# Kernel tuning notes

Measured on AMD Instinct MI355X. Metric: run time of the kernel, lower is better.

The kernel has to match this reference:

```python
import jax, jax.numpy as jnp
import numpy as np

TEMP = 0.07
BASE_TEMP = 0.07


def setup_inputs() -> dict:
    key = jax.random.key(0)
    k1, k2 = jax.random.split(key)
    B, L, D = 512, 20, 128  # batch, num_classes, feat_size
    features = jax.random.normal(k1, (B, L, D), dtype=jnp.float32)
    # contrastive features are typically L2-normalized projections
    features = features / jnp.linalg.norm(features, axis=-1, keepdims=True)
    labels = jax.random.randint(k2, (B, L), 0, 2).astype(jnp.int32)  # multi-hot
    return {"features": features, "labels": labels}


def reference(features, labels):
    # features: [B, L, D], labels: [B, L] multi-hot
    B, L, D = features.shape
    dt = features.dtype
    lab = labels.astype(dt).T                      # [L, B]
    feat = jnp.transpose(features, (1, 0, 2))      # [L, B, D]

    logits_mask = 1.0 - jnp.eye(B, dtype=dt)       # [B, B], zero diagonal
    # mask[c, i, j] = labels[i, c] * labels[j, c] * (i != j)
    mask = (lab[:, :, None] * lab[:, None, :]) * logits_mask  # [L, B, B]

    # anchor_dot_contrast[c, l, i, j] = f[l,i] . f[c,j] / T  -> exp, masked on (i,j)
    # Compute via one big N x N gram, N = L*B (same math, single GEMM).
    F = feat.reshape(L * B, D)
    E = jnp.exp((F @ F.T) / jnp.asarray(TEMP, dt)).reshape(L, B, L, B)  # E[l,i,c,j]
    tot = E.sum(axis=(0, 3))                       # [B(i), L(c)] : sum over l, all j
    diag = jnp.diagonal(E, axis1=1, axis2=3)       # [L(l), L(c), B(i)] : j == i terms
    # sum_exp_logits[c, i] = sum_{l, j != i} exp(f[l,i].f[c,j]/T)
    S = tot.T - diag.sum(axis=0)                   # [L(c), B(i)]

    # numerator[c, i, j] = f[c,i] . f[c,j] / T
    numerator = jnp.einsum('cid,cjd->cij', feat, feat) / jnp.asarray(TEMP, dt)  # [L,B,B]
    log_prob = numerator - jnp.log(S)[:, :, None]  # [L, B, B]

    mean_log_prob_pos = (mask * log_prob).sum(axis=(0, 2))  # [B]
    average = mask.sum(axis=(0, 2))                          # [B]
    average = jnp.where(average == 0, jnp.asarray(1.0, dt), average)
    mean_log_prob_pos = mean_log_prob_pos / average

    loss = -(TEMP / BASE_TEMP) * jnp.mean(mean_log_prob_pos)
    return loss
```

## Files before the change

### kernel.cpp

```cpp
#include <hip/hip_runtime.h>
#include <hip/hip_fp8.h>


#define NB 512
#define NL 20
#define NROW (NB * NL)
#define F8BYTES (NROW * 128)
#define SCALE 4.5398160f
#define TEMP_INV 14.285714285714286f

typedef float f32x4 __attribute__((ext_vector_type(4)));

static __device__ __forceinline__ unsigned char f2fp8(float x) {
  __hip_fp8_e4m3 q(x);
  return (unsigned char)q.__x;
}

static __device__ __forceinline__ float fexp2(float x) {
#if __has_builtin(__builtin_amdgcn_exp2f)
  return __builtin_amdgcn_exp2f(x);
#else
  return exp2f(x);
#endif
}

__global__ __launch_bounds__(256) void k_prep(const float* __restrict__ feat,
                                              const int* __restrict__ labels,
                                              unsigned char* __restrict__ f8,
                                              float* __restrict__ gp) {
  const int b = blockIdx.x;
  if (b < 640) {
    int t = b * 256 + threadIdx.x;
    int q = t & 15;
    int a = t >> 4;
    int l = a >> 9;
    int i = a & 511;
    const float* src = feat + (size_t)i * (NL * 128) + l * 128 + q * 8;
    float4 v0 = *(const float4*)src;
    float4 v1 = *(const float4*)(src + 4);
    unsigned long long u = 0;
    u |= (unsigned long long)f2fp8(v0.x * SCALE);
    u |= (unsigned long long)f2fp8(v0.y * SCALE) << 8;
    u |= (unsigned long long)f2fp8(v0.z * SCALE) << 16;
    u |= (unsigned long long)f2fp8(v0.w * SCALE) << 24;
    u |= (unsigned long long)f2fp8(v1.x * SCALE) << 32;
    u |= (unsigned long long)f2fp8(v1.y * SCALE) << 40;
    u |= (unsigned long long)f2fp8(v1.z * SCALE) << 48;
    u |= (unsigned long long)f2fp8(v1.w * SCALE) << 56;
    *(unsigned long long*)(f8 + (size_t)a * 128 + ((q ^ (a & 15)) << 3)) = u;
  } else {
    __shared__ float part[2][128];
    const int idx = b - 640;
    const int c = idx >> 4, grp = idx & 15;
    const int d = threadIdx.x & 127, half = threadIdx.x >> 7;
    const int i0 = grp * 32 + half * 16;
    float s = 0.f;
#pragma unroll
    for (int k = 0; k < 16; ++k) {
      int i = i0 + k;
      s += (float)labels[i * NL + c] * feat[(size_t)i * (NL * 128) + c * 128 + d];
    }
    part[half][d] = s;
    __syncthreads();
    if (half == 0) gp[(c * 16 + grp) * 128 + d] = part[0][d] + part[1][d];
  }
}

__global__ __launch_bounds__(64) void k_gram(const unsigned char* __restrict__ f8,
                                             float* __restrict__ Pr) {
  __shared__ unsigned char lds[4096];
  const int x = blockIdx.x;
  const int h = x & 1, sr = x >> 1;
  const int c = blockIdx.y;
  const int lane = threadIdx.x;
  const int fr = lane & 15, kg = lane >> 4;
  const int x8 = fr << 3;

  long af[4][4];
#pragma unroll
  for (int kk = 0; kk < 4; ++kk)
#pragma unroll
    for (int m = 0; m < 4; ++m)
      af[kk][m] = *(const long*)(f8 + (size_t)(sr * 64 + m * 16 + fr) * 128 +
                                 ((kk * 32 + kg * 8) ^ x8));

  const unsigned char* gB = f8 + ((size_t)c * 512 + h * 256) * 128 + lane * 16;
  auto stage = [&](int buf, int t) {
    const unsigned char* g = gB + t * 2048;
    unsigned char* lb = lds + buf * 2048 + lane * 16;
    __builtin_amdgcn_global_load_lds(
        (const __attribute__((address_space(1))) unsigned int*)g,
        (__attribute__((address_space(3))) unsigned int*)lb, 16, 0, 0);
    __builtin_amdgcn_global_load_lds(
        (const __attribute__((address_space(1))) unsigned int*)(g + 1024),
        (__attribute__((address_space(3))) unsigned int*)(lb + 1024), 16, 0, 0);
  };

  stage(0, 0);
  float esum[4][4] = {};

  const int d8 = sr & 7;
  const bool diagh = ((d8 >> 2) == h);
  const int td0 = (d8 & 3) * 4;

  for (int t = 0; t < 16; ++t) {
    asm volatile("" ::: "memory");
    if (t < 15) {
      stage((t + 1) & 1, t + 1);
      asm volatile("s_waitcnt vmcnt(2)" ::: "memory");
    } else {
      asm volatile("s_waitcnt vmcnt(0)" ::: "memory");
    }

    const unsigned char* lb = lds + (t & 1) * 2048;
    f32x4 acc[4] = {};
#pragma unroll
    for (int kk = 0; kk < 4; ++kk) {
      long bf = *(const long*)(lb + fr * 128 + ((kk * 32 + kg * 8) ^ x8));
#pragma unroll
      for (int m = 0; m < 4; ++m)
        acc[m] = __builtin_amdgcn_mfma_f32_16x16x32_fp8_fp8(af[kk][m], bf, acc[m], 0, 0, 0);
    }

    if (diagh && t >= td0 && t < td0 + 4) {
      const int mt = t - td0;
#pragma unroll
      for (int m = 0; m < 4; ++m)
#pragma unroll
        for (int reg = 0; reg < 4; ++reg) {
          float ex = fexp2(acc[m][reg]);
          if (m == mt && (kg * 4 + reg) == fr) ex = 0.f;
          esum[m][reg] += ex;
        }
    } else {
#pragma unroll
      for (int m = 0; m < 4; ++m)
#pragma unroll
        for (int reg = 0; reg < 4; ++reg)
          esum[m][reg] += fexp2(acc[m][reg]);
    }
  }

#pragma unroll
  for (int m = 0; m < 4; ++m)
#pragma unroll
    for (int reg = 0; reg < 4; ++reg) {
      float e = esum[m][reg];
      e += __shfl_xor(e, 1, 64); e += __shfl_xor(e, 2, 64);
      e += __shfl_xor(e, 4, 64); e += __shfl_xor(e, 8, 64);
      if (fr == 0)
        Pr[(((size_t)c * 2 + h) * 160 + sr) * 64 + m * 16 + kg * 4 + reg] = e;
    }
}

__global__ __launch_bounds__(256) void k_ws(const float* __restrict__ Pr,
                                            const float* __restrict__ feat,
                                            const float* __restrict__ gp,
                                            float* __restrict__ Slog,
                                            float* __restrict__ wnum) {
  const int b = blockIdx.x;
  if (b < 2560) {
    __shared__ float part[2][128];
    __shared__ float gsh[128];
    const int tid = threadIdx.x;
    const int c = (b * 4) >> 9;
    const int d = tid & 127, qh = tid >> 7;
    float s = 0.f;
#pragma unroll
    for (int q = 0; q < 8; ++q)
      s += gp[(c * 16 + qh * 8 + q) * 128 + d];
    part[qh][d] = s;
    __syncthreads();
    if (tid < 128) gsh[tid] = part[0][tid] + part[1][tid];
    __syncthreads();

    const int lane = tid & 63;
    const int p = b * 4 + (tid >> 6);
    const int i = p & 511;
    float2 f = *(const float2*)(feat + (size_t)i * (NL * 128) + c * 128 + lane * 2);
    float2 gv = *(const float2*)(gsh + lane * 2);
    float v = f.x * gv.x + f.y * gv.y;
#pragma unroll
    for (int sh = 1; sh < 64; sh <<= 1) v += __shfl_xor(v, sh, 64);
    if (lane == 0) wnum[p] = (v - 1.f) * TEMP_INV;
  } else {
    int idx = (b - 2560) * 256 + threadIdx.x;
    int c = idx >> 9, i = idx & 511;
    float s = 0.f;
#pragma unroll
    for (int l2 = 0; l2 < NL; ++l2) {
      const float* p2 = Pr + (((size_t)c * 2) * 160 + l2 * 8 + (i >> 6)) * 64 + (i & 63);
      s += p2[0] + p2[160 * 64];
    }
    Slog[idx] = logf(s);
  }
}

__global__ __launch_bounds__(512) void k_final(const float* __restrict__ Slog,
                                               const float* __restrict__ wnum,
                                               const int* __restrict__ labels,
                                               float* __restrict__ out) {
  __shared__ float cnt[NL];
  __shared__ float red[8];
  const int i = threadIdx.x;
  if (i < NL) cnt[i] = 0.f;
  __syncthreads();
  int lab[NL];
#pragma unroll
  for (int cI = 0; cI < NL; ++cI) lab[cI] = labels[i * NL + cI];
#pragma unroll
  for (int cI = 0; cI < NL; ++cI)
    if (lab[cI]) atomicAdd(&cnt[cI], 1.f);
  __syncthreads();
  float avg = 0.f, acc = 0.f;
#pragma unroll
  for (int cI = 0; cI < NL; ++cI) {
    if (lab[cI]) {
      float wgt = cnt[cI] - 1.f;
      avg += wgt;
      acc += wnum[cI * NB + i] - wgt * Slog[cI * NB + i];
    }
  }
  float v = acc / (avg == 0.f ? 1.f : avg);
#pragma unroll
  for (int s = 1; s < 64; s <<= 1) v += __shfl_xor(v, s, 64);
  if ((i & 63) == 0) red[i >> 6] = v;
  __syncthreads();
  if (i == 0) {
    float tot = 0.f;
#pragma unroll
    for (int k = 0; k < 8; ++k) tot += red[k];
    out[0] = -(tot / (float)NB);
  }
}

extern "C" void kernel_launch(void* const* d_in, const int* in_sizes, int n_in,
                              void* d_out, int out_size, void* d_ws, size_t ws_size,
                              hipStream_t stream) {
  const float* feat = (const float*)d_in[0];
  const int* labels = (const int*)d_in[1];
  float* out = (float*)d_out;
  unsigned char* ws = (unsigned char*)d_ws;
  unsigned char* f8 = ws;
  float* Pr = (float*)(ws + F8BYTES);
  float* gp = Pr + 20 * 2 * 160 * 64;
  float* Slog = gp + 320 * 128;
  float* wnum = Slog + NROW;

  k_prep<<<960, 256, 0, stream>>>(feat, labels, f8, gp);
  dim3 grid(320, 20);
  k_gram<<<grid, 64, 0, stream>>>(f8, Pr);
  k_ws<<<2600, 256, 0, stream>>>(Pr, feat, gp, Slog, wnum);
  k_final<<<1, 512, 0, stream>>>(Slog, wnum, labels, out);
}
```

Before: 51.07 us.

## Fuse log-sum and final reduction into ws kernel with last-block atomic finish

Moves the per-class label counts and per-sample averages into an extra prep block, and folds the Slog computation and the final loss reduction into the ws kernel. Each wave now also reduces its 40 Pr partials with shuffles. Blocks accumulate into 64 atomic buckets, and the last block to finish, found via an atomic counter, writes the output. This removes one kernel launch and the Slog/wnum round trips. In exchange it relies on atomic ordering across blocks and does redundant log work inside wavefronts.

New measurement: 96.62 us. +89.2%, slower.

```diff
diff --git a/kernel.cpp b/kernel.cpp
--- a/kernel.cpp
+++ b/kernel.cpp
@@ -8,6 +8,7 @@
 #define F8BYTES (NROW * 128)
 #define SCALE 4.5398160f
 #define TEMP_INV 14.285714285714286f
+#define WS2_BLOCKS 2560
 
 typedef float f32x4 __attribute__((ext_vector_type(4)));
 
@@ -27,7 +28,11 @@
 __global__ __launch_bounds__(256) void k_prep(const float* __restrict__ feat,
                                               const int* __restrict__ labels,
                                               unsigned char* __restrict__ f8,
-                                              float* __restrict__ gp) {
+                                              float* __restrict__ gp,
+                                              float* __restrict__ avgv,
+                                              float* __restrict__ wgtv,
+                                              float* __restrict__ buckets,
+                                              unsigned int* __restrict__ ctr) {
   const int b = blockIdx.x;
   if (b < 640) {
     int t = b * 256 + threadIdx.x;
@@ -48,7 +53,7 @@
     u |= (unsigned long long)f2fp8(v1.z * SCALE) << 48;
     u |= (unsigned long long)f2fp8(v1.w * SCALE) << 56;
     *(unsigned long long*)(f8 + (size_t)a * 128 + ((q ^ (a & 15)) << 3)) = u;
-  } else {
+  } else if (b < 960) {
     __shared__ float part[2][128];
     const int idx = b - 640;
     const int c = idx >> 4, grp = idx & 15;
@@ -63,6 +68,34 @@
     part[half][d] = s;
     __syncthreads();
     if (half == 0) gp[(c * 16 + grp) * 128 + d] = part[0][d] + part[1][d];
+  } else {
+    __shared__ float cnt[NL];
+    const int tid = threadIdx.x;
+    if (tid < NL) cnt[tid] = 0.f;
+    if (tid >= 32 && tid < 96) buckets[tid - 32] = 0.f;
+    if (tid == 96) *ctr = 0u;
+    __syncthreads();
+    int lab2[2][NL];
+#pragma unroll
+    for (int hh = 0; hh < 2; ++hh)
+#pragma unroll
+      for (int cI = 0; cI < NL; ++cI)
+        lab2[hh][cI] = labels[(tid + hh * 256) * NL + cI];
+#pragma unroll
+    for (int hh = 0; hh < 2; ++hh)
+#pragma unroll
+      for (int cI = 0; cI < NL; ++cI)
+        if (lab2[hh][cI]) atomicAdd(&cnt[cI], 1.f);
+    __syncthreads();
+#pragma unroll
+    for (int hh = 0; hh < 2; ++hh) {
+      float av = 0.f;
+#pragma unroll
+      for (int cI = 0; cI < NL; ++cI)
+        av += lab2[hh][cI] ? (cnt[cI] - 1.f) : 0.f;
+      avgv[tid + hh * 256] = av;
+    }
+    if (tid < NL) wgtv[tid] = cnt[tid] - 1.f;
   }
 }
 
@@ -153,84 +186,66 @@
     }
 }
 
-__global__ __launch_bounds__(256) void k_ws(const float* __restrict__ Pr,
-                                            const float* __restrict__ feat,
-                                            const float* __restrict__ gp,
-                                            float* __restrict__ Slog,
-                                            float* __restrict__ wnum) {
+__global__ __launch_bounds__(256) void k_ws2(const float* __restrict__ Pr,
+                                             const float* __restrict__ feat,
+                                             const float* __restrict__ gp,
+                                             const int* __restrict__ labels,
+                                             const float* __restrict__ avgv,
+                                             const float* __restrict__ wgtv,
+                                             float* __restrict__ buckets,
+                                             unsigned int* __restrict__ ctr,
+                                             float* __restrict__ out) {
+  __shared__ float part[2][128];
+  __shared__ float gsh[128];
+  __shared__ float termsh[4];
   const int b = blockIdx.x;
-  if (b < 2560) {
-    __shared__ float part[2][128];
-    __shared__ float gsh[128];
-    const int tid = threadIdx.x;
-    const int c = (b * 4) >> 9;
-    const int d = tid & 127, qh = tid >> 7;
-    float s = 0.f;
-#pragma unroll
-    for (int q = 0; q < 8; ++q)
-      s += gp[(c * 16 + qh * 8 + q) * 128 + d];
-    part[qh][d] = s;
-    __syncthreads();
-    if (tid < 128) gsh[tid] = part[0][tid] + part[1][tid];
-    __syncthreads();
-
-    const int lane = tid & 63;
-    const int p = b * 4 + (tid >> 6);
-    const int i = p & 511;
-    float2 f = *(const float2*)(feat + (size_t)i * (NL * 128) + c * 128 + lane * 2);
-    float2 gv = *(const float2*)(gsh + lane * 2);
-    float v = f.x * gv.x + f.y * gv.y;
-#pragma unroll
-    for (int sh = 1; sh < 64; sh <<= 1) v += __shfl_xor(v, sh, 64);
-    if (lane == 0) wnum[p] = (v - 1.f) * TEMP_INV;
-  } else {
-    int idx = (b - 2560) * 256 + threadIdx.x;
-    int c = idx >> 9, i = idx & 511;
-    float s = 0.f;
-#pragma unroll
-    for (int l2 = 0; l2 < NL; ++l2) {
-      const float* p2 = Pr + (((size_t)c * 2) * 160 + l2 * 8 + (i >> 6)) * 64 + (i & 63);
-      s += p2[0] + p2[160 * 64];
-    }
-    Slog[idx] = logf(s);
-  }
-}
-
-__global__ __launch_bounds__(512) void k_final(const float* __restrict__ Slog,
-                                               const float* __restrict__ wnum,
-                                               const int* __restrict__ labels,
-                                               float* __restrict__ out) {
-  __shared__ float cnt[NL];
-  __shared__ float red[8];
-  const int i = threadIdx.x;
-  if (i < NL) cnt[i] = 0.f;
+  const int tid = threadIdx.x;
+  const int c = (b * 4) >> 9;
+  const int d = tid & 127, qh = tid >> 7;
+  float s0 = 0.f;
+#pragma unroll
+  for (int q = 0; q < 8; ++q)
+    s0 += gp[(c * 16 + qh * 8 + q) * 128 + d];
+  part[qh][d] = s0;
   __syncthreads();
-  int lab[NL];
-#pragma unroll
-  for (int cI = 0; cI < NL; ++cI) lab[cI] = labels[i * NL + cI];
-#pragma unroll
-  for (int cI = 0; cI < NL; ++cI)
-    if (lab[cI]) atomicAdd(&cnt[cI], 1.f);
+  if (tid < 128) gsh[tid] = part[0][tid] + part[1][tid];
   __syncthreads();
-  float avg = 0.f, acc = 0.f;
-#pragma unroll
-  for (int cI = 0; cI < NL; ++cI) {
-    if (lab[cI]) {
-      float wgt = cnt[cI] - 1.f;
-      avg += wgt;
-      acc += wnum[cI * NB + i] - wgt * Slog[cI * NB + i];
-    }
-  }
-  float v = acc / (avg == 0.f ? 1.f : avg);
-#pragma unroll
-  for (int s = 1; s < 64; s <<= 1) v += __shfl_xor(v, s, 64);
-  if ((i & 63) == 0) red[i >> 6] = v;
+
+  const int lane = tid & 63, w = tid >> 6;
+  const int p = b * 4 + w;
+  const int i = p & 511;
+  float2 f = *(const float2*)(feat + (size_t)i * (NL * 128) + c * 128 + lane * 2);
+  float2 gv = *(const float2*)(gsh + lane * 2);
+  float v = f.x * gv.x + f.y * gv.y;
+  float sp = 0.f;
+  if (lane < 40) {
+    const int l2 = lane >> 1, hp = lane & 1;
+    sp = Pr[(((size_t)c * 2 + hp) * 160 + l2 * 8 + (i >> 6)) * 64 + (i & 63)];
+  }
+#pragma unroll
+  for (int sh = 1; sh < 64; sh <<= 1) {
+    v += __shfl_xor(v, sh, 64);
+    sp += __shfl_xor(sp, sh, 64);
+  }
+  if (lane == 0) {
+    const float wnum = (v - 1.f) * TEMP_INV;
+    const int lab = labels[i * NL + c];
+    float term = 0.f;
+    if (lab) term = wnum - wgtv[c] * logf(sp);
+    const float av = avgv[i];
+    termsh[w] = term / (av == 0.f ? 1.f : av);
+  }
   __syncthreads();
-  if (i == 0) {
-    float tot = 0.f;
-#pragma unroll
-    for (int k = 0; k < 8; ++k) tot += red[k];
-    out[0] = -(tot / (float)NB);
+  if (tid == 0) {
+    const float t4 = termsh[0] + termsh[1] + termsh[2] + termsh[3];
+    atomicAdd(&buckets[b & 63], t4);
+    asm volatile("s_waitcnt vmcnt(0)" ::: "memory");
+    const unsigned int old = atomicAdd(ctr, 1u);
+    if (old == WS2_BLOCKS - 1) {
+      float tot = 0.f;
+      for (int k = 0; k < 64; ++k) tot += atomicAdd(&buckets[k], 0.f);
+      out[0] = -(tot / (float)NB);
+    }
   }
 }
 
@@ -244,12 +259,14 @@
   unsigned char* f8 = ws;
   float* Pr = (float*)(ws + F8BYTES);
   float* gp = Pr + 20 * 2 * 160 * 64;
-  float* Slog = gp + 320 * 128;
-  float* wnum = Slog + NROW;
-
-  k_prep<<<960, 256, 0, stream>>>(feat, labels, f8, gp);
+  float* avgv = gp + 320 * 128;
+  float* wgtv = avgv + NB;
+  float* buckets = wgtv + 32;
+  unsigned int* ctr = (unsigned int*)(buckets + 64);
+
+  k_prep<<<961, 256, 0, stream>>>(feat, labels, f8, gp, avgv, wgtv, buckets, ctr);
   dim3 grid(320, 20);
   k_gram<<<grid, 64, 0, stream>>>(f8, Pr);
-  k_ws<<<2600, 256, 0, stream>>>(Pr, feat, gp, Slog, wnum);
-  k_final<<<1, 512, 0, stream>>>(Slog, wnum, labels, out);
-}
+  k_ws2<<<WS2_BLOCKS, 256, 0, stream>>>(Pr, feat, gp, labels, avgv, wgtv,
+                                        buckets, ctr, out);
+}
```
